# Kernel optimization log

Measured on AMD Instinct MI355X. Metric: run time of the kernel, lower is better.

Reference implementation:

```python
import jax, jax.numpy as jnp
import numpy as np

OUT_F = 8192
IN_F = 8192
RANK = 32
N_TOK = 128


def _pack_ternary(w_q):
    """Pack int8 ternary {-1,0,+1} [out,in] -> uint8 [out,in//4], LSB-first 2-bit codes."""
    enc = (w_q.astype(np.int32) + 1).astype(np.uint8).reshape(w_q.shape[0], -1, 4)
    packed = enc[:, :, 0] | (enc[:, :, 1] << 2) | (enc[:, :, 2] << 4) | (enc[:, :, 3] << 6)
    return packed


def setup_inputs() -> dict:
    key = jax.random.key(0)
    kx, kw, ks, ka, kb, kbias = jax.random.split(key, 6)
    x = jax.random.normal(kx, (N_TOK, IN_F), dtype=jnp.float32)
    # ternary weights in {-1,0,+1}
    w_q = np.asarray(jax.random.randint(kw, (OUT_F, IN_F), -1, 2, dtype=jnp.int32), dtype=np.int8)
    weight_packed = jnp.asarray(_pack_ternary(w_q), dtype=jnp.uint8)
    scale = jax.random.uniform(ks, (OUT_F,), dtype=jnp.float32, minval=0.01, maxval=0.05)
    lora_A = jax.random.normal(ka, (OUT_F, RANK), dtype=jnp.float32) * 0.02
    lora_B = jax.random.normal(kb, (RANK, IN_F), dtype=jnp.float32) * 0.02
    bias = jax.random.normal(kbias, (OUT_F,), dtype=jnp.float32) * 0.01
    return {"x": x, "weight_packed": weight_packed, "scale": scale,
            "lora_A": lora_A, "lora_B": lora_B, "bias": bias, "in_features": IN_F}


def _unpack_ternary(packed, in_features, dtype):
    # packed: uint8 [out, in//4]; LSB-first 2-bit codes, code-1 -> {-1,0,+1}
    p = packed.astype(jnp.int32)
    vals = jnp.stack([p & 3, (p >> 2) & 3, (p >> 4) & 3, (p >> 6) & 3], axis=-1)
    vals = vals.reshape(packed.shape[0], -1)[:, :in_features] - 1
    return vals.astype(dtype)


def reference(x, weight_packed, scale, lora_A, lora_B, bias, in_features):
    W = _unpack_ternary(weight_packed, in_features, x.dtype)  # [out, in]
    out = (x @ W.T) * scale[None, :]                          # [n, out]
    out = out + (x @ lora_B.T) @ lora_A.T                     # low-rank LoRA path
    out = out + bias
    return out
```

## Files before the change

### kernel.cpp

```cpp
#include <hip/hip_runtime.h>
#include <hip/hip_bf16.h>
#include <stdint.h>

typedef float f32x4 __attribute__((ext_vector_type(4)));
typedef __bf16 bf16x8 __attribute__((ext_vector_type(8)));
typedef unsigned short ushort8 __attribute__((ext_vector_type(8)));

#define N_TOK 128
#define OUT_F 8192
#define IN_F  8192
#define RANK  32

#define KSPLIT 16
#define KB    (IN_F / KSPLIT)
#define BK    64
#define NSTEP (KB / BK)
#define WSTRIDE 16
#define LKC   4

#define XB_OFF 0
#define TB_OFF ((size_t)N_TOK * IN_F * 2)
#define PO_OFF (TB_OFF + (size_t)LKC * N_TOK * RANK * 4)

__device__ __forceinline__ unsigned short bf16r(float f) {
    uint32_t u = __float_as_uint(f);
    return (unsigned short)((u + 0x7FFFu + ((u >> 16) & 1u)) >> 16);
}

__device__ __forceinline__ int swz(int row, int col) { return col ^ ((row & 7) << 3); }

__global__ __launch_bounds__(256) void cvt_x(const float* __restrict__ x,
                                             unsigned short* __restrict__ xt) {
    size_t f = (size_t)blockIdx.x * 256 + threadIdx.x;
    int lane = (int)(f & 63);
    int rec  = (int)(f >> 6);
    int ar16 = rec & 7;
    int kk   = (rec >> 3) & 1;
    int sblk = rec >> 4;
    int row = ar16 * 16 + (lane & 15);
    int k   = sblk * 64 + kk * 32 + (lane >> 4) * 8;
    const float4* sp = (const float4*)(x + (size_t)row * IN_F + k);
    float4 a = sp[0], b = sp[1];
    ushort8 o;
    o[0] = bf16r(a.x); o[1] = bf16r(a.y); o[2] = bf16r(a.z); o[3] = bf16r(a.w);
    o[4] = bf16r(b.x); o[5] = bf16r(b.y); o[6] = bf16r(b.z); o[7] = bf16r(b.w);
    *(ushort8*)(xt + f * 8) = o;
}

__global__ __launch_bounds__(256) void lora_t(const float* __restrict__ x,
                                              const float* __restrict__ lb,
                                              float* __restrict__ tB) {
    __shared__ float ts[256][33];
    __shared__ float ps[8][32];
    const int m = blockIdx.x >> 2, kc = blockIdx.x & 3;
    const int tid = threadIdx.x;
    const int c0 = kc * 2048 + tid * 8;
    float4 xv0 = *(const float4*)(x + (size_t)m * IN_F + c0);
    float4 xv1 = *(const float4*)(x + (size_t)m * IN_F + c0 + 4);
#pragma unroll
    for (int r = 0; r < RANK; ++r) {
        const float4* bp = (const float4*)(lb + (size_t)r * IN_F + c0);
        float4 b0 = bp[0], b1 = bp[1];
        float s = xv0.x * b0.x + xv0.y * b0.y + xv0.z * b0.z + xv0.w * b0.w +
                  xv1.x * b1.x + xv1.y * b1.y + xv1.z * b1.z + xv1.w * b1.w;
        ts[tid][r] = s;
    }
    __syncthreads();
    {
        int g = tid >> 5, r = tid & 31;
        float s = 0.f;
        for (int j = 0; j < 32; ++j) s += ts[g * 32 + j][r];
        ps[g][r] = s;
    }
    __syncthreads();
    if (tid < 32) {
        float s = 0.f;
#pragma unroll
        for (int g = 0; g < 8; ++g) s += ps[g][tid];
        tB[(kc * N_TOK + m) * RANK + tid] = s;
    }
}

__device__ __forceinline__ void decodeW(int4 v, uint32_t d[8]) {
    uint32_t p = (uint32_t)v.x | ((uint32_t)v.y << 8) |
                 ((uint32_t)v.z << 16) | ((uint32_t)v.w << 24);
    const uint32_t HI = 0x403F00BFu;
    const uint32_t LO = 0x00800080u;
#pragma unroll
    for (int j = 0; j < 8; ++j) {
        uint32_t c0 = (p >> (4 * j)) & 3u;
        uint32_t c1 = (p >> (4 * j + 2)) & 3u;
        uint32_t t = c0 | (c1 << 16);
        uint32_t sel = (t | (t << 8)) + 0x04000400u;
        d[j] = __builtin_amdgcn_perm(HI, LO, sel);
    }
}

__global__ __launch_bounds__(256, 3) void ternary_gemm(const unsigned short* __restrict__ xt,
                                                       const int* __restrict__ wp,
                                                       unsigned short* __restrict__ pO) {
    __shared__ unsigned short ww[2][128][64];
    const int tid = threadIdx.x;
    const int nb = blockIdx.x >> 4;
    const int ks = blockIdx.x & 15;
    const int n0 = nb * 128;
    const int lane = tid & 63;
    const int wid = tid >> 6;
    const int wr = wid >> 1, wc = wid & 1;

    const int srow = tid >> 2;
    const int xcol = (tid & 3) * 16;
    const int* pg0 = wp + (size_t)(n0 + srow) * (IN_F / 4) + ks * (KB / 4) + (tid & 3) * 4;
    const int* pg1 = pg0 + (size_t)64 * (IN_F / 4);

    const int arow = lane & 15;
    const int kgrp = (lane >> 4) * 8;
    const int wc0 = swz(srow, xcol), wc1 = swz(srow, xcol + 8);

    const unsigned short* abase = xt + ((size_t)(ks * NSTEP) * 16) * 512 + lane * 8;
#define LDA(s_, kk_, ar_) \
    (*(const bf16x8*)(abase + ((size_t)((s_)*16 + (kk_)*8 + (wr * 4 + (ar_)))) * 512))

    f32x4 acc[4][4];
#pragma unroll
    for (int i = 0; i < 4; ++i)
#pragma unroll
        for (int j = 0; j < 4; ++j) acc[i][j] = (f32x4){0.f, 0.f, 0.f, 0.f};

    int4 wP[2][2];

    wP[0][0] = *(const int4*)(pg0);
    wP[0][1] = *(const int4*)(pg1);
    wP[1][0] = *(const int4*)(pg0 + WSTRIDE);
    wP[1][1] = *(const int4*)(pg1 + WSTRIDE);
    {
        uint32_t d0[8], d1[8];
        decodeW(wP[0][0], d0);
        decodeW(wP[0][1], d1);
        *(uint4*)&ww[0][srow][wc0]      = make_uint4(d0[0], d0[1], d0[2], d0[3]);
        *(uint4*)&ww[0][srow][wc1]      = make_uint4(d0[4], d0[5], d0[6], d0[7]);
        *(uint4*)&ww[0][srow + 64][wc0] = make_uint4(d1[0], d1[1], d1[2], d1[3]);
        *(uint4*)&ww[0][srow + 64][wc1] = make_uint4(d1[4], d1[5], d1[6], d1[7]);
    }
    wP[0][0] = *(const int4*)(pg0 + 2 * WSTRIDE);
    wP[0][1] = *(const int4*)(pg1 + 2 * WSTRIDE);
    __builtin_amdgcn_sched_barrier(0);
    asm volatile("s_waitcnt lgkmcnt(0)" ::: "memory");
    __builtin_amdgcn_s_barrier();
    __builtin_amdgcn_sched_barrier(0);

#pragma unroll
    for (int s = 0; s < NSTEP; ++s) {
        const int cur = s & 1, nxt = cur ^ 1;
#pragma unroll
        for (int kk = 0; kk < 2; ++kk) {
            bf16x8 aK[4], bfr[4];
#pragma unroll
            for (int ar = 0; ar < 4; ++ar) aK[ar] = LDA(s, kk, ar);
#pragma unroll
            for (int br = 0; br < 4; ++br) {
                int row = wc * 64 + br * 16 + arow;
                bfr[br] = *(const bf16x8*)&ww[cur][row][swz(row, kk * 32 + kgrp)];
            }
#pragma unroll
            for (int ar = 0; ar < 4; ++ar)
#pragma unroll
                for (int br = 0; br < 4; ++br)
                    acc[ar][br] = __builtin_amdgcn_mfma_f32_16x16x32_bf16(
                        aK[ar], bfr[br], acc[ar][br], 0, 0, 0);
        }
        if (s + 1 < NSTEP) {
            uint32_t d0[8], d1[8];
            decodeW(wP[nxt][0], d0);
            decodeW(wP[nxt][1], d1);
            *(uint4*)&ww[nxt][srow][wc0]      = make_uint4(d0[0], d0[1], d0[2], d0[3]);
            *(uint4*)&ww[nxt][srow][wc1]      = make_uint4(d0[4], d0[5], d0[6], d0[7]);
            *(uint4*)&ww[nxt][srow + 64][wc0] = make_uint4(d1[0], d1[1], d1[2], d1[3]);
            *(uint4*)&ww[nxt][srow + 64][wc1] = make_uint4(d1[4], d1[5], d1[6], d1[7]);
            if (s + 3 < NSTEP) {
                wP[nxt][0] = *(const int4*)(pg0 + (s + 3) * WSTRIDE);
                wP[nxt][1] = *(const int4*)(pg1 + (s + 3) * WSTRIDE);
            }
            __builtin_amdgcn_sched_barrier(0);
            asm volatile("s_waitcnt lgkmcnt(0)" ::: "memory");
            __builtin_amdgcn_s_barrier();
            __builtin_amdgcn_sched_barrier(0);
        }
    }
#undef LDA

    unsigned short* po = pO + ((size_t)ks << 20);
    const int mrow = (lane >> 4) * 4;
#pragma unroll
    for (int ar = 0; ar < 4; ++ar) {
#pragma unroll
        for (int br = 0; br < 4; ++br) {
            int m = wr * 64 + ar * 16 + mrow;
            int n = n0 + wc * 64 + br * 16 + arow;
            unsigned short* pp = po + (size_t)m * OUT_F + n;
#pragma unroll
            for (int j = 0; j < 4; ++j) pp[(size_t)j * OUT_F] = bf16r(acc[ar][br][j]);
        }
    }
}

__global__ __launch_bounds__(256) void reduce_out(const unsigned short* __restrict__ pO,
                                                  const float* __restrict__ tB,
                                                  const float* __restrict__ scale,
                                                  const float* __restrict__ lora_A,
                                                  const float* __restrict__ bias,
                                                  float* __restrict__ out) {
    __shared__ float ts[4][RANK];
    int nb = blockIdx.x & 15, mg = blockIdx.x >> 4;
    int tid = threadIdx.x;
    int m0 = mg * 4;
    if (tid < 128) {
        int i = tid >> 5, r = tid & 31;
        float s = 0.f;
#pragma unroll
        for (int c = 0; c < LKC; ++c) s += tB[(c * N_TOK + m0 + i) * RANK + r];
        ts[i][r] = s;
    }
    __syncthreads();
    int n = nb * 512 + tid * 2;
    float sc0 = scale[n], sc1 = scale[n + 1];
    float bs0 = bias[n], bs1 = bias[n + 1];
    float4 a0[8], a1[8];
    const float4* ap0 = (const float4*)(lora_A + (size_t)n * RANK);
    const float4* ap1 = (const float4*)(lora_A + (size_t)(n + 1) * RANK);
#pragma unroll
    for (int q = 0; q < 8; ++q) { a0[q] = ap0[q]; a1[q] = ap1[q]; }
#pragma unroll
    for (int i = 0; i < 4; ++i) {
        int m = m0 + i;
        const unsigned short* pp = pO + (size_t)m * OUT_F + n;
        float s0 = 0.f, s1 = 0.f;
#pragma unroll
        for (int c = 0; c < KSPLIT; ++c) {
            uint32_t u = *(const uint32_t*)(pp + ((size_t)c << 20));
            s0 += __uint_as_float(u << 16);
            s1 += __uint_as_float(u & 0xFFFF0000u);
        }
        float l0 = 0.f, l1 = 0.f;
#pragma unroll
        for (int q = 0; q < 8; ++q) {
            float4 tv = *(const float4*)&ts[i][q * 4];
            l0 = fmaf(tv.x, a0[q].x, l0); l0 = fmaf(tv.y, a0[q].y, l0);
            l0 = fmaf(tv.z, a0[q].z, l0); l0 = fmaf(tv.w, a0[q].w, l0);
            l1 = fmaf(tv.x, a1[q].x, l1); l1 = fmaf(tv.y, a1[q].y, l1);
            l1 = fmaf(tv.z, a1[q].z, l1); l1 = fmaf(tv.w, a1[q].w, l1);
        }
        out[(size_t)m * OUT_F + n]     = fmaf(s0, sc0, l0 + bs0);
        out[(size_t)m * OUT_F + n + 1] = fmaf(s1, sc1, l1 + bs1);
    }
}

extern "C" void kernel_launch(void* const* d_in, const int* in_sizes, int n_in,
                              void* d_out, int out_size, void* d_ws, size_t ws_size,
                              hipStream_t stream) {
    const float* x      = (const float*)d_in[0];
    const int*   wp     = (const int*)d_in[1];
    const float* scale  = (const float*)d_in[2];
    const float* lora_A = (const float*)d_in[3];
    const float* lora_B = (const float*)d_in[4];
    const float* bias   = (const float*)d_in[5];
    float* out = (float*)d_out;

    char* ws = (char*)d_ws;
    unsigned short* xt = (unsigned short*)(ws + XB_OFF);
    float* tB = (float*)(ws + TB_OFF);
    unsigned short* pO = (unsigned short*)(ws + PO_OFF);

    cvt_x<<<512, 256, 0, stream>>>(x, xt);
    lora_t<<<N_TOK * LKC, 256, 0, stream>>>(x, lora_B, tB);
    ternary_gemm<<<(OUT_F / 128) * KSPLIT, 256, 0, stream>>>(xt, wp, pO);
    reduce_out<<<16 * 32, 256, 0, stream>>>(pO, tB, scale, lora_A, bias, out);
}
```

Before: 56.16 us.

## Replace split-K partial buffer and reduce kernel with atomic accumulation into output

The split-K GEMM now scales its accumulators and atomically adds fp32 results directly into the output, which a new lora_out kernel pre-initializes with the LoRA term plus bias. This removes the bf16 partial-output workspace round trip and the separate reduction pass. KSPLIT is halved to 8, which cuts the number of atomic contributions per element but also halves the grid to 512 blocks. The occupancy hint on launch_bounds is dropped. Float atomics make the summation order nondeterministic, and the atomic traffic may contend.

```diff
diff --git a/kernel.cpp b/kernel.cpp
--- a/kernel.cpp
+++ b/kernel.cpp
@@ -11,7 +11,7 @@
 #define IN_F  8192
 #define RANK  32
 
-#define KSPLIT 16
+#define KSPLIT 8
 #define KB    (IN_F / KSPLIT)
 #define BK    64
 #define NSTEP (KB / BK)
@@ -20,7 +20,6 @@
 
 #define XB_OFF 0
 #define TB_OFF ((size_t)N_TOK * IN_F * 2)
-#define PO_OFF (TB_OFF + (size_t)LKC * N_TOK * RANK * 4)
 
 __device__ __forceinline__ unsigned short bf16r(float f) {
     uint32_t u = __float_as_uint(f);
@@ -81,6 +80,46 @@
     }
 }
 
+__global__ __launch_bounds__(256) void lora_out(const float* __restrict__ tB,
+                                                const float* __restrict__ lora_A,
+                                                const float* __restrict__ bias,
+                                                float* __restrict__ out) {
+    __shared__ float ts[4][RANK];
+    int nb = blockIdx.x & 15, mg = blockIdx.x >> 4;
+    int tid = threadIdx.x;
+    int m0 = mg * 4;
+    if (tid < 128) {
+        int i = tid >> 5, r = tid & 31;
+        float s = 0.f;
+#pragma unroll
+        for (int c = 0; c < LKC; ++c) s += tB[(c * N_TOK + m0 + i) * RANK + r];
+        ts[i][r] = s;
+    }
+    __syncthreads();
+    int n = nb * 512 + tid * 2;
+    float bs0 = bias[n], bs1 = bias[n + 1];
+    float4 a0[8], a1[8];
+    const float4* ap0 = (const float4*)(lora_A + (size_t)n * RANK);
+    const float4* ap1 = (const float4*)(lora_A + (size_t)(n + 1) * RANK);
+#pragma unroll
+    for (int q = 0; q < 8; ++q) { a0[q] = ap0[q]; a1[q] = ap1[q]; }
+#pragma unroll
+    for (int i = 0; i < 4; ++i) {
+        int m = m0 + i;
+        float l0 = 0.f, l1 = 0.f;
+#pragma unroll
+        for (int q = 0; q < 8; ++q) {
+            float4 tv = *(const float4*)&ts[i][q * 4];
+            l0 = fmaf(tv.x, a0[q].x, l0); l0 = fmaf(tv.y, a0[q].y, l0);
+            l0 = fmaf(tv.z, a0[q].z, l0); l0 = fmaf(tv.w, a0[q].w, l0);
+            l1 = fmaf(tv.x, a1[q].x, l1); l1 = fmaf(tv.y, a1[q].y, l1);
+            l1 = fmaf(tv.z, a1[q].z, l1); l1 = fmaf(tv.w, a1[q].w, l1);
+        }
+        out[(size_t)m * OUT_F + n]     = l0 + bs0;
+        out[(size_t)m * OUT_F + n + 1] = l1 + bs1;
+    }
+}
+
 __device__ __forceinline__ void decodeW(int4 v, uint32_t d[8]) {
     uint32_t p = (uint32_t)v.x | ((uint32_t)v.y << 8) |
                  ((uint32_t)v.z << 16) | ((uint32_t)v.w << 24);
@@ -96,13 +135,14 @@
     }
 }
 
-__global__ __launch_bounds__(256, 3) void ternary_gemm(const unsigned short* __restrict__ xt,
-                                                       const int* __restrict__ wp,
-                                                       unsigned short* __restrict__ pO) {
+__global__ __launch_bounds__(256) void ternary_gemm(const unsigned short* __restrict__ xt,
+                                                    const int* __restrict__ wp,
+                                                    const float* __restrict__ scale,
+                                                    float* __restrict__ out) {
     __shared__ unsigned short ww[2][128][64];
     const int tid = threadIdx.x;
-    const int nb = blockIdx.x >> 4;
-    const int ks = blockIdx.x & 15;
+    const int nb = blockIdx.x >> 3;
+    const int ks = blockIdx.x & 7;
     const int n0 = nb * 128;
     const int lane = tid & 63;
     const int wid = tid >> 6;
@@ -189,69 +229,19 @@
     }
 #undef LDA
 
-    unsigned short* po = pO + ((size_t)ks << 20);
     const int mrow = (lane >> 4) * 4;
 #pragma unroll
-    for (int ar = 0; ar < 4; ++ar) {
-#pragma unroll
-        for (int br = 0; br < 4; ++br) {
+    for (int br = 0; br < 4; ++br) {
+        int n = n0 + wc * 64 + br * 16 + arow;
+        float sc = scale[n];
+#pragma unroll
+        for (int ar = 0; ar < 4; ++ar) {
             int m = wr * 64 + ar * 16 + mrow;
-            int n = n0 + wc * 64 + br * 16 + arow;
-            unsigned short* pp = po + (size_t)m * OUT_F + n;
-#pragma unroll
-            for (int j = 0; j < 4; ++j) pp[(size_t)j * OUT_F] = bf16r(acc[ar][br][j]);
-        }
-    }
-}
-
-__global__ __launch_bounds__(256) void reduce_out(const unsigned short* __restrict__ pO,
-                                                  const float* __restrict__ tB,
-                                                  const float* __restrict__ scale,
-                                                  const float* __restrict__ lora_A,
-                                                  const float* __restrict__ bias,
-                                                  float* __restrict__ out) {
-    __shared__ float ts[4][RANK];
-    int nb = blockIdx.x & 15, mg = blockIdx.x >> 4;
-    int tid = threadIdx.x;
-    int m0 = mg * 4;
-    if (tid < 128) {
-        int i = tid >> 5, r = tid & 31;
-        float s = 0.f;
-#pragma unroll
-        for (int c = 0; c < LKC; ++c) s += tB[(c * N_TOK + m0 + i) * RANK + r];
-        ts[i][r] = s;
-    }
-    __syncthreads();
-    int n = nb * 512 + tid * 2;
-    float sc0 = scale[n], sc1 = scale[n + 1];
-    float bs0 = bias[n], bs1 = bias[n + 1];
-    float4 a0[8], a1[8];
-    const float4* ap0 = (const float4*)(lora_A + (size_t)n * RANK);
-    const float4* ap1 = (const float4*)(lora_A + (size_t)(n + 1) * RANK);
-#pragma unroll
-    for (int q = 0; q < 8; ++q) { a0[q] = ap0[q]; a1[q] = ap1[q]; }
-#pragma unroll
-    for (int i = 0; i < 4; ++i) {
-        int m = m0 + i;
-        const unsigned short* pp = pO + (size_t)m * OUT_F + n;
-        float s0 = 0.f, s1 = 0.f;
-#pragma unroll
-        for (int c = 0; c < KSPLIT; ++c) {
-            uint32_t u = *(const uint32_t*)(pp + ((size_t)c << 20));
-            s0 += __uint_as_float(u << 16);
-            s1 += __uint_as_float(u & 0xFFFF0000u);
-        }
-        float l0 = 0.f, l1 = 0.f;
-#pragma unroll
-        for (int q = 0; q < 8; ++q) {
-            float4 tv = *(const float4*)&ts[i][q * 4];
-            l0 = fmaf(tv.x, a0[q].x, l0); l0 = fmaf(tv.y, a0[q].y, l0);
-            l0 = fmaf(tv.z, a0[q].z, l0); l0 = fmaf(tv.w, a0[q].w, l0);
-            l1 = fmaf(tv.x, a1[q].x, l1); l1 = fmaf(tv.y, a1[q].y, l1);
-            l1 = fmaf(tv.z, a1[q].z, l1); l1 = fmaf(tv.w, a1[q].w, l1);
-        }
-        out[(size_t)m * OUT_F + n]     = fmaf(s0, sc0, l0 + bs0);
-        out[(size_t)m * OUT_F + n + 1] = fmaf(s1, sc1, l1 + bs1);
+            float* pp = out + (size_t)m * OUT_F + n;
+#pragma unroll
+            for (int j = 0; j < 4; ++j)
+                unsafeAtomicAdd(pp + (size_t)j * OUT_F, acc[ar][br][j] * sc);
+        }
     }
 }
 
@@ -269,10 +259,9 @@
     char* ws = (char*)d_ws;
     unsigned short* xt = (unsigned short*)(ws + XB_OFF);
     float* tB = (float*)(ws + TB_OFF);
-    unsigned short* pO = (unsigned short*)(ws + PO_OFF);
 
     cvt_x<<<512, 256, 0, stream>>>(x, xt);
     lora_t<<<N_TOK * LKC, 256, 0, stream>>>(x, lora_B, tB);
-    ternary_gemm<<<(OUT_F / 128) * KSPLIT, 256, 0, stream>>>(xt, wp, pO);
-    reduce_out<<<16 * 32, 256, 0, stream>>>(pO, tB, scale, lora_A, bias, out);
-}
+    lora_out<<<16 * 32, 256, 0, stream>>>(tB, lora_A, bias, out);
+    ternary_gemm<<<(OUT_F / 128) * KSPLIT, 256, 0, stream>>>(xt, wp, scale, out);
+}
```

After: 68.97 us. 1.23x slower.

## Halve split-K factor and restructure main loop as rolled ping-pong pairs

Applied to the files above, without the earlier changes.

Reduces the split-K factor from 16 to 8, so each block handles twice as many K steps and fewer partial outputs go to the reduction. The fully unrolled step loop becomes a non-unrolled loop over pairs of steps with explicit double-buffer slots, and the occupancy hint in launch bounds is dropped. The aim is to cut partial-sum write and reduce traffic and code size. The grid halves, though, which may leave CUs underused, and reduce_out must still match the new KSPLIT.

```diff
diff --git a/kernel.cpp b/kernel.cpp
--- a/kernel.cpp
+++ b/kernel.cpp
@@ -11,7 +11,7 @@
 #define IN_F  8192
 #define RANK  32
 
-#define KSPLIT 16
+#define KSPLIT 8
 #define KB    (IN_F / KSPLIT)
 #define BK    64
 #define NSTEP (KB / BK)
@@ -96,13 +96,13 @@
     }
 }
 
-__global__ __launch_bounds__(256, 3) void ternary_gemm(const unsigned short* __restrict__ xt,
-                                                       const int* __restrict__ wp,
-                                                       unsigned short* __restrict__ pO) {
+__global__ __launch_bounds__(256) void ternary_gemm(const unsigned short* __restrict__ xt,
+                                                    const int* __restrict__ wp,
+                                                    unsigned short* __restrict__ pO) {
     __shared__ unsigned short ww[2][128][64];
     const int tid = threadIdx.x;
-    const int nb = blockIdx.x >> 4;
-    const int ks = blockIdx.x & 15;
+    const int nb = blockIdx.x >> 3;
+    const int ks = blockIdx.x & 7;
     const int n0 = nb * 128;
     const int lane = tid & 63;
     const int wid = tid >> 6;
@@ -121,73 +121,85 @@
 #define LDA(s_, kk_, ar_) \
     (*(const bf16x8*)(abase + ((size_t)((s_)*16 + (kk_)*8 + (wr * 4 + (ar_)))) * 512))
 
+#define STAGE_WW(wreg0, wreg1, buf_)                                              \
+    {                                                                             \
+        uint32_t d0[8], d1[8];                                                    \
+        decodeW((wreg0), d0);                                                     \
+        decodeW((wreg1), d1);                                                     \
+        *(uint4*)&ww[(buf_)][srow][wc0]      = make_uint4(d0[0], d0[1], d0[2], d0[3]); \
+        *(uint4*)&ww[(buf_)][srow][wc1]      = make_uint4(d0[4], d0[5], d0[6], d0[7]); \
+        *(uint4*)&ww[(buf_)][srow + 64][wc0] = make_uint4(d1[0], d1[1], d1[2], d1[3]); \
+        *(uint4*)&ww[(buf_)][srow + 64][wc1] = make_uint4(d1[4], d1[5], d1[6], d1[7]); \
+    }
+
+#define MFMA_STEP(s_, buf_)                                                       \
+    {                                                                             \
+        _Pragma("unroll")                                                         \
+        for (int kk = 0; kk < 2; ++kk) {                                          \
+            bf16x8 aK[4], bfr[4];                                                 \
+            _Pragma("unroll")                                                     \
+            for (int ar = 0; ar < 4; ++ar) aK[ar] = LDA((s_), kk, ar);            \
+            _Pragma("unroll")                                                     \
+            for (int br = 0; br < 4; ++br) {                                      \
+                int row = wc * 64 + br * 16 + arow;                               \
+                bfr[br] = *(const bf16x8*)&ww[(buf_)][row][swz(row, kk * 32 + kgrp)]; \
+            }                                                                     \
+            _Pragma("unroll")                                                     \
+            for (int ar = 0; ar < 4; ++ar)                                        \
+                _Pragma("unroll")                                                 \
+                for (int br = 0; br < 4; ++br)                                    \
+                    acc[ar][br] = __builtin_amdgcn_mfma_f32_16x16x32_bf16(        \
+                        aK[ar], bfr[br], acc[ar][br], 0, 0, 0);                   \
+        }                                                                         \
+    }
+
+#define LGKM_BARRIER                                                              \
+    __builtin_amdgcn_sched_barrier(0);                                            \
+    asm volatile("s_waitcnt lgkmcnt(0)" ::: "memory");                            \
+    __builtin_amdgcn_s_barrier();                                                 \
+    __builtin_amdgcn_sched_barrier(0);
+
     f32x4 acc[4][4];
 #pragma unroll
     for (int i = 0; i < 4; ++i)
 #pragma unroll
         for (int j = 0; j < 4; ++j) acc[i][j] = (f32x4){0.f, 0.f, 0.f, 0.f};
 
-    int4 wP[2][2];
-
-    wP[0][0] = *(const int4*)(pg0);
-    wP[0][1] = *(const int4*)(pg1);
-    wP[1][0] = *(const int4*)(pg0 + WSTRIDE);
-    wP[1][1] = *(const int4*)(pg1 + WSTRIDE);
-    {
-        uint32_t d0[8], d1[8];
-        decodeW(wP[0][0], d0);
-        decodeW(wP[0][1], d1);
-        *(uint4*)&ww[0][srow][wc0]      = make_uint4(d0[0], d0[1], d0[2], d0[3]);
-        *(uint4*)&ww[0][srow][wc1]      = make_uint4(d0[4], d0[5], d0[6], d0[7]);
-        *(uint4*)&ww[0][srow + 64][wc0] = make_uint4(d1[0], d1[1], d1[2], d1[3]);
-        *(uint4*)&ww[0][srow + 64][wc1] = make_uint4(d1[4], d1[5], d1[6], d1[7]);
-    }
-    wP[0][0] = *(const int4*)(pg0 + 2 * WSTRIDE);
-    wP[0][1] = *(const int4*)(pg1 + 2 * WSTRIDE);
-    __builtin_amdgcn_sched_barrier(0);
-    asm volatile("s_waitcnt lgkmcnt(0)" ::: "memory");
-    __builtin_amdgcn_s_barrier();
-    __builtin_amdgcn_sched_barrier(0);
-
-#pragma unroll
-    for (int s = 0; s < NSTEP; ++s) {
-        const int cur = s & 1, nxt = cur ^ 1;
-#pragma unroll
-        for (int kk = 0; kk < 2; ++kk) {
-            bf16x8 aK[4], bfr[4];
-#pragma unroll
-            for (int ar = 0; ar < 4; ++ar) aK[ar] = LDA(s, kk, ar);
-#pragma unroll
-            for (int br = 0; br < 4; ++br) {
-                int row = wc * 64 + br * 16 + arow;
-                bfr[br] = *(const bf16x8*)&ww[cur][row][swz(row, kk * 32 + kgrp)];
+    int4 w0a, w0b, w1a, w1b;
+
+    w0a = *(const int4*)(pg0);
+    w0b = *(const int4*)(pg1);
+    w1a = *(const int4*)(pg0 + WSTRIDE);
+    w1b = *(const int4*)(pg1 + WSTRIDE);
+    STAGE_WW(w0a, w0b, 0);
+    w0a = *(const int4*)(pg0 + 2 * WSTRIDE);
+    w0b = *(const int4*)(pg1 + 2 * WSTRIDE);
+    LGKM_BARRIER;
+
+#pragma unroll 1
+    for (int sp = 0; sp < NSTEP / 2; ++sp) {
+        const int s0 = 2 * sp, s1 = 2 * sp + 1;
+        MFMA_STEP(s0, 0);
+        STAGE_WW(w1a, w1b, 1);
+        if (s0 + 3 < NSTEP) {
+            w1a = *(const int4*)(pg0 + (s0 + 3) * WSTRIDE);
+            w1b = *(const int4*)(pg1 + (s0 + 3) * WSTRIDE);
+        }
+        LGKM_BARRIER;
+        MFMA_STEP(s1, 1);
+        if (s1 + 1 < NSTEP) {
+            STAGE_WW(w0a, w0b, 0);
+            if (s1 + 3 < NSTEP) {
+                w0a = *(const int4*)(pg0 + (s1 + 3) * WSTRIDE);
+                w0b = *(const int4*)(pg1 + (s1 + 3) * WSTRIDE);
             }
-#pragma unroll
-            for (int ar = 0; ar < 4; ++ar)
-#pragma unroll
-                for (int br = 0; br < 4; ++br)
-                    acc[ar][br] = __builtin_amdgcn_mfma_f32_16x16x32_bf16(
-                        aK[ar], bfr[br], acc[ar][br], 0, 0, 0);
-        }
-        if (s + 1 < NSTEP) {
-            uint32_t d0[8], d1[8];
-            decodeW(wP[nxt][0], d0);
-            decodeW(wP[nxt][1], d1);
-            *(uint4*)&ww[nxt][srow][wc0]      = make_uint4(d0[0], d0[1], d0[2], d0[3]);
-            *(uint4*)&ww[nxt][srow][wc1]      = make_uint4(d0[4], d0[5], d0[6], d0[7]);
-            *(uint4*)&ww[nxt][srow + 64][wc0] = make_uint4(d1[0], d1[1], d1[2], d1[3]);
-            *(uint4*)&ww[nxt][srow + 64][wc1] = make_uint4(d1[4], d1[5], d1[6], d1[7]);
-            if (s + 3 < NSTEP) {
-                wP[nxt][0] = *(const int4*)(pg0 + (s + 3) * WSTRIDE);
-                wP[nxt][1] = *(const int4*)(pg1 + (s + 3) * WSTRIDE);
-            }
-            __builtin_amdgcn_sched_barrier(0);
-            asm volatile("s_waitcnt lgkmcnt(0)" ::: "memory");
-            __builtin_amdgcn_s_barrier();
-            __builtin_amdgcn_sched_barrier(0);
+            LGKM_BARRIER;
         }
     }
 #undef LDA
+#undef STAGE_WW
+#undef MFMA_STEP
+#undef LGKM_BARRIER
 
     unsigned short* po = pO + ((size_t)ks << 20);
     const int mrow = (lane >> 4) * 4;
```

Result: slower. 59.43 us (+5.8%).

## Halve K-split and prefetch packed weights in groups of four steps

Applied to the files above, without the earlier changes.

Reduces the K-split from 16 to 8, so each block handles twice as many K steps and fewer partial outputs are written and reduced. Packed weight loads are now issued in batches of four steps into two alternating register groups, so more global loads are in flight well before they are decoded into LDS. The launch-bounds occupancy hint is dropped, which lets the compiler use more registers for the larger prefetch buffers but may lower occupancy and halves the grid size. The reduce kernel must also be consistent with the new split count, presumably through the shared macro.

```diff
diff --git a/kernel.cpp b/kernel.cpp
--- a/kernel.cpp
+++ b/kernel.cpp
@@ -11,7 +11,7 @@
 #define IN_F  8192
 #define RANK  32
 
-#define KSPLIT 16
+#define KSPLIT 8
 #define KB    (IN_F / KSPLIT)
 #define BK    64
 #define NSTEP (KB / BK)
@@ -96,13 +96,13 @@
     }
 }
 
-__global__ __launch_bounds__(256, 3) void ternary_gemm(const unsigned short* __restrict__ xt,
-                                                       const int* __restrict__ wp,
-                                                       unsigned short* __restrict__ pO) {
+__global__ __launch_bounds__(256) void ternary_gemm(const unsigned short* __restrict__ xt,
+                                                    const int* __restrict__ wp,
+                                                    unsigned short* __restrict__ pO) {
     __shared__ unsigned short ww[2][128][64];
     const int tid = threadIdx.x;
-    const int nb = blockIdx.x >> 4;
-    const int ks = blockIdx.x & 15;
+    const int nb = blockIdx.x >> 3;
+    const int ks = blockIdx.x & 7;
     const int n0 = nb * 128;
     const int lane = tid & 63;
     const int wid = tid >> 6;
@@ -127,27 +127,40 @@
 #pragma unroll
         for (int j = 0; j < 4; ++j) acc[i][j] = (f32x4){0.f, 0.f, 0.f, 0.f};
 
-    int4 wP[2][2];
-
-    wP[0][0] = *(const int4*)(pg0);
-    wP[0][1] = *(const int4*)(pg1);
-    wP[1][0] = *(const int4*)(pg0 + WSTRIDE);
-    wP[1][1] = *(const int4*)(pg1 + WSTRIDE);
-    {
-        uint32_t d0[8], d1[8];
-        decodeW(wP[0][0], d0);
-        decodeW(wP[0][1], d1);
-        *(uint4*)&ww[0][srow][wc0]      = make_uint4(d0[0], d0[1], d0[2], d0[3]);
-        *(uint4*)&ww[0][srow][wc1]      = make_uint4(d0[4], d0[5], d0[6], d0[7]);
-        *(uint4*)&ww[0][srow + 64][wc0] = make_uint4(d1[0], d1[1], d1[2], d1[3]);
-        *(uint4*)&ww[0][srow + 64][wc1] = make_uint4(d1[4], d1[5], d1[6], d1[7]);
-    }
-    wP[0][0] = *(const int4*)(pg0 + 2 * WSTRIDE);
-    wP[0][1] = *(const int4*)(pg1 + 2 * WSTRIDE);
+    int4 wgA[4][2], wgB[4][2];
+
+#define LOAD_GROUP(buf_, g_)                                                      \
+    {                                                                             \
+        __builtin_amdgcn_sched_barrier(0);                                        \
+        _Pragma("unroll")                                                         \
+        for (int j = 0; j < 4; ++j) {                                             \
+            buf_[j][0] = *(const int4*)(pg0 + ((g_)*4 + j) * WSTRIDE);            \
+            buf_[j][1] = *(const int4*)(pg1 + ((g_)*4 + j) * WSTRIDE);            \
+        }                                                                         \
+        __builtin_amdgcn_sched_barrier(0);                                        \
+    }
+
+#define STAGE_WW(w0_, w1_, buf_)                                                  \
+    {                                                                             \
+        uint32_t d0[8], d1[8];                                                    \
+        decodeW((w0_), d0);                                                       \
+        decodeW((w1_), d1);                                                       \
+        *(uint4*)&ww[(buf_)][srow][wc0]      = make_uint4(d0[0], d0[1], d0[2], d0[3]); \
+        *(uint4*)&ww[(buf_)][srow][wc1]      = make_uint4(d0[4], d0[5], d0[6], d0[7]); \
+        *(uint4*)&ww[(buf_)][srow + 64][wc0] = make_uint4(d1[0], d1[1], d1[2], d1[3]); \
+        *(uint4*)&ww[(buf_)][srow + 64][wc1] = make_uint4(d1[4], d1[5], d1[6], d1[7]); \
+    }
+
+#define LGKM_BARRIER                                                              \
+    __builtin_amdgcn_sched_barrier(0);                                            \
+    asm volatile("s_waitcnt lgkmcnt(0)" ::: "memory");                            \
+    __builtin_amdgcn_s_barrier();                                                 \
     __builtin_amdgcn_sched_barrier(0);
-    asm volatile("s_waitcnt lgkmcnt(0)" ::: "memory");
-    __builtin_amdgcn_s_barrier();
-    __builtin_amdgcn_sched_barrier(0);
+
+    LOAD_GROUP(wgA, 0);
+    LOAD_GROUP(wgB, 1);
+    STAGE_WW(wgA[0][0], wgA[0][1], 0);
+    LGKM_BARRIER;
 
 #pragma unroll
     for (int s = 0; s < NSTEP; ++s) {
@@ -169,25 +182,23 @@
                     acc[ar][br] = __builtin_amdgcn_mfma_f32_16x16x32_bf16(
                         aK[ar], bfr[br], acc[ar][br], 0, 0, 0);
         }
+        if ((s & 3) == 3 && (s >> 2) + 2 < NSTEP / 4) {
+            const int gn = (s >> 2) + 2;
+            if (gn & 1) { LOAD_GROUP(wgB, gn); }
+            else        { LOAD_GROUP(wgA, gn); }
+        }
         if (s + 1 < NSTEP) {
-            uint32_t d0[8], d1[8];
-            decodeW(wP[nxt][0], d0);
-            decodeW(wP[nxt][1], d1);
-            *(uint4*)&ww[nxt][srow][wc0]      = make_uint4(d0[0], d0[1], d0[2], d0[3]);
-            *(uint4*)&ww[nxt][srow][wc1]      = make_uint4(d0[4], d0[5], d0[6], d0[7]);
-            *(uint4*)&ww[nxt][srow + 64][wc0] = make_uint4(d1[0], d1[1], d1[2], d1[3]);
-            *(uint4*)&ww[nxt][srow + 64][wc1] = make_uint4(d1[4], d1[5], d1[6], d1[7]);
-            if (s + 3 < NSTEP) {
-                wP[nxt][0] = *(const int4*)(pg0 + (s + 3) * WSTRIDE);
-                wP[nxt][1] = *(const int4*)(pg1 + (s + 3) * WSTRIDE);
-            }
-            __builtin_amdgcn_sched_barrier(0);
-            asm volatile("s_waitcnt lgkmcnt(0)" ::: "memory");
-            __builtin_amdgcn_s_barrier();
-            __builtin_amdgcn_sched_barrier(0);
+            const int sn = s + 1;
+            const int jn = sn & 3;
+            if ((sn >> 2) & 1) { STAGE_WW(wgB[jn][0], wgB[jn][1], nxt); }
+            else               { STAGE_WW(wgA[jn][0], wgA[jn][1], nxt); }
+            LGKM_BARRIER;
         }
     }
 #undef LDA
+#undef LOAD_GROUP
+#undef STAGE_WW
+#undef LGKM_BARRIER
 
     unsigned short* po = pO + ((size_t)ks << 20);
     const int mrow = (lane >> 4) * 4;
```

New measurement: 55.79 us. Within noise of the previous version (-0.7%).
